# Kernel optimization log

Hardware: AMD Instinct MI355X
Metric: run time of the kernel (lower is better)

## Reference

```python
import jax, jax.numpy as jnp
import numpy as np
import math

B, S, D, H = 2, 2048, 1024, 16
DH = D // H
FF = 4096
EPS = 1e-5


def _xavier(k, shape):
    lim = math.sqrt(6.0 / (shape[0] + shape[1]))
    return jax.random.uniform(k, shape, jnp.float32, -lim, lim)


def setup_inputs() -> dict:
    key = jax.random.key(0)
    ks = jax.random.split(key, 8)
    return {
        "x": jax.random.normal(ks[0], (B, S, D), jnp.float32),
        "mask": jnp.ones((B, S), jnp.int32),
        "WQ": _xavier(ks[1], (D, D)), "bQ": jnp.zeros((D,), jnp.float32),
        "WK": _xavier(ks[2], (D, D)), "bK": jnp.zeros((D,), jnp.float32),
        "WV": _xavier(ks[3], (D, D)), "bV": jnp.zeros((D,), jnp.float32),
        "WY": _xavier(ks[4], (D, D)), "bY": jnp.zeros((D,), jnp.float32),
        "ln1_w": jnp.ones((D,), jnp.float32), "ln1_b": jnp.zeros((D,), jnp.float32),
        "ln2_w": jnp.ones((D,), jnp.float32), "ln2_b": jnp.zeros((D,), jnp.float32),
        "W1": _xavier(ks[5], (D, FF)), "b1": jnp.zeros((FF,), jnp.float32),
        "W2": _xavier(ks[6], (FF, D)), "b2": jnp.zeros((D,), jnp.float32),
    }


def _layer_norm(x, w, b):
    # manual LayerNorm: biased variance over last dim
    m = jnp.mean(x, axis=-1, keepdims=True)
    v = jnp.mean(jnp.square(x - m), axis=-1, keepdims=True)
    return (x - m) / jnp.sqrt(v + EPS) * w + b


def _attention(x, mask, WQ, bQ, WK, bK, WV, bV, WY, bY):
    b, s, _ = x.shape
    def split(t):  # (B,S,D) -> (B,H,S,DH)
        return t.reshape(b, s, H, DH).transpose(0, 2, 1, 3)
    q = split(x @ WQ + bQ)
    k = split(x @ WK + bK)
    v = split(x @ WV + bV)
    scores = jnp.einsum('bhqd,bhkd->bhqk', q, k) / math.sqrt(DH)
    scores = jnp.where(mask[:, None, None, :] == 0, -jnp.inf, scores)
    w = jax.nn.softmax(scores, axis=-1)
    y = jnp.einsum('bhqk,bhkd->bhqd', w, v)
    y = y.transpose(0, 2, 1, 3).reshape(b, s, D)  # merge heads
    return y @ WY + bY


def reference(x, mask, WQ, bQ, WK, bK, WV, bV, WY, bY,
              ln1_w, ln1_b, ln2_w, ln2_b, W1, b1, W2, b2):
    a = _attention(x, mask, WQ, bQ, WK, bK, WV, bV, WY, bY)
    h = _layer_norm(a + x, ln1_w, ln1_b)
    ff = jax.nn.gelu(h @ W1 + b1, approximate=False) @ W2 + b2
    return _layer_norm(ff + h, ln2_w, ln2_b)
```

## Files before the change

### kernel.cpp

```cpp
#include <hip/hip_runtime.h>
#include <cstdint>
#include <cstddef>

#define B_ 2
#define S_ 2048
#define D_ 1024
#define H_ 16
#define DH_ 64
#define FF_ 4096
#define M_ (B_*S_)
#define MB_ ((size_t)1 << 20)
#define NT_ (S_/64)

using u16 = unsigned short;
using u64 = unsigned long long;
using short8 = __attribute__((ext_vector_type(8))) short;
using short4v = __attribute__((ext_vector_type(4))) short;
using floatx4 = __attribute__((ext_vector_type(4))) float;
using u64x2 = __attribute__((ext_vector_type(2))) unsigned long long;

__device__ __forceinline__ float bf2f(u16 u) {
    return __uint_as_float(((uint32_t)u) << 16);
}
__device__ __forceinline__ u16 f2bf(float f) {
    uint32_t u = __float_as_uint(f);
    u += 0x7fffu + ((u >> 16) & 1u);
    return (u16)(u >> 16);
}
__device__ __forceinline__ uint32_t cvtpk_bf16(float lo, float hi) {
    uint32_t r;
    asm("v_cvt_pk_bf16_f32 %0, %1, %2" : "=v"(r) : "v"(lo), "v"(hi));
    return r;
}
__device__ __forceinline__ void async_copy16(const u16* g, u16* l) {
    __builtin_amdgcn_global_load_lds(
        (const __attribute__((address_space(1))) uint32_t*)g,
        (__attribute__((address_space(3))) uint32_t*)l, 16, 0, 0);
}

__device__ __forceinline__ float gelu_f(float v) {
    const float ax = fabsf(v) * 0.70710678118f;
    const float t  = __builtin_amdgcn_rcpf(fmaf(0.3275911f, ax, 1.f));
    float p = fmaf(1.061405429f, t, -1.453152027f);
    p = fmaf(p, t, 1.421413741f);
    p = fmaf(p, t, -0.284496736f);
    p = fmaf(p, t, 0.254829592f);
    p *= t;
    const float e = __builtin_amdgcn_exp2f(ax * ax * -1.4426950408889634f);
    float erfv = fmaf(-p, e, 1.f);
    erfv = copysignf(erfv, v);
    return 0.5f * v * (1.f + erfv);
}

__device__ __forceinline__ int swz_inv(int l) {
    return (l & 56) | ((l - (l >> 3)) & 7);
}
__device__ __forceinline__ int swz_fwd(int b) {
    return (b & 56) | ((b + (b >> 3)) & 7);
}

__device__ __forceinline__ void stage4(const u16* gA, const u16* gB,
                                       u16* lA, u16* lB, int w, int K) {
    async_copy16(gA, lA + w * 512);
    async_copy16(gA + (size_t)64 * K, lA + w * 512 + 2048);
    async_copy16(gB, lB + w * 512);
    async_copy16(gB + (size_t)64 * K, lB + w * 512 + 2048);
}

__device__ __forceinline__ void gemm_core(
    const u16* gA, const u16* gB, int K, int nk,
    u16 (&As)[3][128 * 32], u16 (&Bs)[3][128 * 32],
    int w, int wm, int wn, int lm, int quad, floatx4 (&acc)[4][4])
{
    const int pblk = swz_fwd(lm * 4 + quad);

    stage4(gA, gB, As[0], Bs[0], w, K); gA += 32; gB += 32;
    stage4(gA, gB, As[1], Bs[1], w, K); gA += 32; gB += 32;
    asm volatile("s_waitcnt vmcnt(4)" ::: "memory");
    __builtin_amdgcn_s_barrier();

    int cur = 0, stg = 2;
    for (int t = 0; t < nk; ++t) {
        if (t + 2 < nk) {
            stage4(gA, gB, As[stg], Bs[stg], w, K);
            gA += 32; gB += 32;
        }
        const u16* Ac = As[cur];
        const u16* Bc = Bs[cur];
        short8 af[4], bfr[4];
#pragma unroll
        for (int t4 = 0; t4 < 4; ++t4)
            af[t4] = *(const short8*)&Ac[(wm * 4 + t4) * 512 + pblk * 8];
#pragma unroll
        for (int t4 = 0; t4 < 4; ++t4)
            bfr[t4] = *(const short8*)&Bc[(wn * 4 + t4) * 512 + pblk * 8];
#pragma unroll
        for (int i = 0; i < 4; ++i)
#pragma unroll
            for (int j = 0; j < 4; ++j)
                acc[i][j] = __builtin_amdgcn_mfma_f32_16x16x32_bf16(
                    af[i], bfr[j], acc[i][j], 0, 0, 0);

        if (t + 2 < nk)      asm volatile("s_waitcnt vmcnt(4)" ::: "memory");
        else if (t + 1 < nk) asm volatile("s_waitcnt vmcnt(0)" ::: "memory");
        if (t + 1 < nk) __builtin_amdgcn_s_barrier();
        cur = (cur == 2) ? 0 : cur + 1;
        stg = (stg == 2) ? 0 : stg + 1;
    }
}

__global__ __launch_bounds__(256) void cvt_f32_bf16(
    const float* __restrict__ in, u16* __restrict__ out, int n)
{
    const int i = (blockIdx.x * 256 + threadIdx.x) * 4;
    if (i < n) {
        const float4 v = *(const float4*)(in + i);
        out[i + 0] = f2bf(v.x);
        out[i + 1] = f2bf(v.y);
        out[i + 2] = f2bf(v.z);
        out[i + 3] = f2bf(v.w);
    }
}

__global__ __launch_bounds__(256) void mask_bias(
    const int* __restrict__ mask, float* __restrict__ bias, int n)
{
    const int i = blockIdx.x * 256 + threadIdx.x;
    if (i < n) bias[i] = mask[i] ? 0.f : -1e30f;
}

__global__ void transpose_cvt(const float* __restrict__ in, u16* __restrict__ out,
                              int R, int C) {
    __shared__ float t[32][33];
    const int bx = blockIdx.x * 32, by = blockIdx.y * 32;
    const int tx = threadIdx.x, ty = threadIdx.y;
#pragma unroll
    for (int i = 0; i < 32; i += 8)
        t[ty + i][tx] = in[(size_t)(by + ty + i) * C + bx + tx];
    __syncthreads();
#pragma unroll
    for (int i = 0; i < 32; i += 8)
        out[(size_t)(bx + ty + i) * R + by + tx] = f2bf(t[tx][ty + i]);
}

__global__ void transpose_cvt4(
    const float* __restrict__ WQ, const float* __restrict__ WK,
    const float* __restrict__ WV, const float* __restrict__ WY,
    u16* __restrict__ Wqkvt, u16* __restrict__ WYt)
{
    __shared__ float t[32][33];
    const int zz = blockIdx.z;
    const float* in = zz == 0 ? WQ : zz == 1 ? WK : zz == 2 ? WV : WY;
    u16* out = zz < 3 ? Wqkvt + (size_t)zz * D_ * D_ : WYt;
    const int bx = blockIdx.x * 32, by = blockIdx.y * 32;
    const int tx = threadIdx.x, ty = threadIdx.y;
#pragma unroll
    for (int i = 0; i < 32; i += 8)
        t[ty + i][tx] = in[(size_t)(by + ty + i) * D_ + bx + tx];
    __syncthreads();
#pragma unroll
    for (int i = 0; i < 32; i += 8)
        out[(size_t)(bx + ty + i) * D_ + by + tx] = f2bf(t[tx][ty + i]);
}

template<bool GELU, bool OUT_F32>
__global__ __launch_bounds__(256) void gemm_bt(
    const u16* __restrict__ A, const u16* __restrict__ Bt,
    const float* __restrict__ bias, void* __restrict__ Cout,
    int M, int N, int K)
{
    __shared__ alignas(16) u16 As[3][128 * 32];
    __shared__ alignas(16) u16 Bs[3][128 * 32];
    const int tid = threadIdx.x;
    const int w = tid >> 6, lane = tid & 63;
    const int lm = lane & 15, quad = lane >> 4;
    const int wm = w >> 1, wn = w & 1;

    const int nwg = gridDim.x * gridDim.y;
    int bid = blockIdx.y * gridDim.x + blockIdx.x;
    if ((nwg & 7) == 0) {
        const int cpx = nwg >> 3;
        bid = (bid & 7) * cpx + (bid >> 3);
    }
    const int bx = bid % gridDim.x, by = bid / gridDim.x;
    const size_t m0 = (size_t)by * 128, n0 = (size_t)bx * 128;

    const int bwr = swz_inv(lane);
    const int rowS = w * 16 + (bwr >> 2);
    const int colS = (bwr & 3) * 8;
    const u16* gA = A + (m0 + rowS) * K + colS;
    const u16* gB = Bt + (n0 + rowS) * K + colS;

    floatx4 acc[4][4];
    const floatx4 z = {0.f, 0.f, 0.f, 0.f};
#pragma unroll
    for (int i = 0; i < 4; ++i)
#pragma unroll
        for (int j = 0; j < 4; ++j) acc[i][j] = z;

    gemm_core(gA, gB, K, K >> 5, As, Bs, w, wm, wn, lm, quad, acc);

#pragma unroll
    for (int i = 0; i < 4; ++i) {
        const size_t r0 = m0 + wm * 64 + i * 16 + quad * 4;
#pragma unroll
        for (int j = 0; j < 4; ++j) {
            const size_t c = n0 + wn * 64 + j * 16 + lm;
            const float bv = bias[c];
#pragma unroll
            for (int t = 0; t < 4; ++t) {
                float v = acc[i][j][t] + bv;
                if (GELU) v = gelu_f(v);
                if (OUT_F32) ((float*)Cout)[(r0 + t) * (size_t)N + c] = v;
                else         ((u16*)Cout)[(r0 + t) * (size_t)N + c] = f2bf(v);
            }
        }
    }
}

__global__ __launch_bounds__(256) void gemm_bt_skp(
    const u16* __restrict__ A, const u16* __restrict__ Bt,
    const float* __restrict__ bias, float* __restrict__ out0,
    float* __restrict__ Pext, int M, int N, int K)
{
    __shared__ alignas(16) u16 As[3][128 * 32];
    __shared__ alignas(16) u16 Bs[3][128 * 32];
    const int tid = threadIdx.x;
    const int w = tid >> 6, lane = tid & 63;
    const int lm = lane & 15, quad = lane >> 4;
    const int wm = w >> 1, wn = w & 1;
    const int kh = blockIdx.z;
    const int Ks = K / gridDim.z;

    const int nwg = gridDim.x * gridDim.y;
    int bid = blockIdx.y * gridDim.x + blockIdx.x;
    if ((nwg & 7) == 0) {
        const int cpx = nwg >> 3;
        bid = (bid & 7) * cpx + (bid >> 3);
    }
    const int bx = bid % gridDim.x, by = bid / gridDim.x;
    const size_t m0 = (size_t)by * 128, n0 = (size_t)bx * 128;

    const int bwr = swz_inv(lane);
    const int rowS = w * 16 + (bwr >> 2);
    const int colS = (bwr & 3) * 8;
    const u16* gA = A + (m0 + rowS) * K + (size_t)kh * Ks + colS;
    const u16* gB = Bt + (n0 + rowS) * K + (size_t)kh * Ks + colS;

    floatx4 acc[4][4];
    const floatx4 z = {0.f, 0.f, 0.f, 0.f};
#pragma unroll
    for (int i = 0; i < 4; ++i)
#pragma unroll
        for (int j = 0; j < 4; ++j) acc[i][j] = z;

    gemm_core(gA, gB, K, Ks >> 5, As, Bs, w, wm, wn, lm, quad, acc);

    float* Cout = (kh == 0) ? out0 : Pext + (size_t)(kh - 1) * ((size_t)M * N);
#pragma unroll
    for (int i = 0; i < 4; ++i) {
        const size_t r0 = m0 + wm * 64 + i * 16 + quad * 4;
#pragma unroll
        for (int j = 0; j < 4; ++j) {
            const size_t c = n0 + wn * 64 + j * 16 + lm;
            const float bv = (kh == 0) ? bias[c] : 0.f;
#pragma unroll
            for (int t = 0; t < 4; ++t)
                Cout[(r0 + t) * (size_t)N + c] = acc[i][j][t] + bv;
        }
    }
}

__global__ __launch_bounds__(256) void gemm_bt_sk2(
    const u16* __restrict__ A, const u16* __restrict__ Bt,
    const float* __restrict__ bias, float* __restrict__ Cout,
    int M, int N, int K)
{
    __shared__ alignas(16) u16 As[3][128 * 32];
    __shared__ alignas(16) u16 Bs[3][128 * 32];
    const int tid = threadIdx.x;
    const int w = tid >> 6, lane = tid & 63;
    const int lm = lane & 15, quad = lane >> 4;
    const int wm = w >> 1, wn = w & 1;
    const int kh = blockIdx.z;
    const int Ks = K >> 1;
    const size_t m0 = (size_t)blockIdx.y * 128, n0 = (size_t)blockIdx.x * 128;

    const int bwr = swz_inv(lane);
    const int rowS = w * 16 + (bwr >> 2);
    const int colS = (bwr & 3) * 8;
    const u16* gA = A + (m0 + rowS) * K + (size_t)kh * Ks + colS;
    const u16* gB = Bt + (n0 + rowS) * K + (size_t)kh * Ks + colS;

    floatx4 acc[4][4];
    const floatx4 z = {0.f, 0.f, 0.f, 0.f};
#pragma unroll
    for (int i = 0; i < 4; ++i)
#pragma unroll
        for (int j = 0; j < 4; ++j) acc[i][j] = z;

    gemm_core(gA, gB, K, Ks >> 5, As, Bs, w, wm, wn, lm, quad, acc);

#pragma unroll
    for (int i = 0; i < 4; ++i) {
        const size_t r0 = m0 + wm * 64 + i * 16 + quad * 4;
#pragma unroll
        for (int j = 0; j < 4; ++j) {
            const size_t c = n0 + wn * 64 + j * 16 + lm;
            const float bv = (kh == 0) ? bias[c] : 0.f;
#pragma unroll
            for (int t = 0; t < 4; ++t)
                atomicAdd(&Cout[(r0 + t) * (size_t)N + c], acc[i][j][t] + bv);
        }
    }
}

__global__ __launch_bounds__(256) void gemm_qkv(
    const u16* __restrict__ A, const u16* __restrict__ Bt,
    const float* __restrict__ bQ, const float* __restrict__ bK,
    const float* __restrict__ bV,
    u16* __restrict__ Qb, u16* __restrict__ Kb, u16* __restrict__ Vt)
{
    const int K = D_;
    __shared__ alignas(16) u16 As[3][128 * 32];
    __shared__ alignas(16) u16 Bs[3][128 * 32];
    const int tid = threadIdx.x;
    const int w = tid >> 6, lane = tid & 63;
    const int lm = lane & 15, quad = lane >> 4;
    const int wm = w >> 1, wn = w & 1;

    const int nwg = gridDim.x * gridDim.y;
    int bid = blockIdx.y * gridDim.x + blockIdx.x;
    if ((nwg & 7) == 0) {
        const int cpx = nwg >> 3;
        bid = (bid & 7) * cpx + (bid >> 3);
    }
    const int bx = bid % gridDim.x, by = bid / gridDim.x;
    const size_t m0 = (size_t)by * 128, n0 = (size_t)bx * 128;

    const int bwr = swz_inv(lane);
    const int rowS = w * 16 + (bwr >> 2);
    const int colS = (bwr & 3) * 8;
    const u16* gA = A + (m0 + rowS) * K + colS;
    const u16* gB = Bt + (n0 + rowS) * K + colS;

    floatx4 acc[4][4];
    const floatx4 z = {0.f, 0.f, 0.f, 0.f};
#pragma unroll
    for (int i = 0; i < 4; ++i)
#pragma unroll
        for (int j = 0; j < 4; ++j) acc[i][j] = z;

    gemm_core(gA, gB, K, K >> 5, As, Bs, w, wm, wn, lm, quad, acc);

#pragma unroll
    for (int i = 0; i < 4; ++i) {
        const size_t r0 = m0 + wm * 64 + i * 16 + quad * 4;
#pragma unroll
        for (int j = 0; j < 4; ++j) {
            const size_t c = n0 + wn * 64 + j * 16 + lm;
            const int sel = (int)(c >> 10);
            const int col = (int)(c & 1023);
            const float bv = sel == 0 ? bQ[col] : (sel == 1 ? bK[col] : bV[col]);
#pragma unroll
            for (int t = 0; t < 4; ++t) {
                const size_t r = r0 + t;
                const u16 v = f2bf(acc[i][j][t] + bv);
                if (sel == 0)      Qb[r * (size_t)D_ + col] = v;
                else if (sel == 1) Kb[r * (size_t)D_ + col] = v;
                else {
                    const int h = col >> 6, dh = col & 63;
                    const int bb = (int)(r >> 11), s = (int)(r & 2047);
                    Vt[((size_t)((bb * 16 + h) * 64 + dh)) * S_ + s] = v;
                }
            }
        }
    }
}

__global__ __launch_bounds__(256) void attn_kernel(
    const u16* __restrict__ Q, const u16* __restrict__ Kg,
    const u16* __restrict__ Vt, const float* __restrict__ mbias,
    u16* __restrict__ O)
{
    __shared__ alignas(16) u16 Kt[2][64 * 72];
    __shared__ alignas(16) u16 Vs[2][64 * 72];
    const int tid = threadIdx.x, w = tid >> 6, lane = tid & 63;
    const int lm = lane & 15, quad = lane >> 4;
    const int b = blockIdx.y >> 4, h = blockIdx.y & 15;
    const int q0 = blockIdx.x * 64;

    const u16* qp = Q + ((size_t)(b * S_ + q0 + w * 16 + lm)) * D_ + h * 64;
    const short8 bq0 = *(const short8*)(qp + quad * 8);
    const short8 bq1 = *(const short8*)(qp + 32 + quad * 8);

    const int sRow = tid >> 2, sCol = (tid & 3) * 16;
    const int wswz = (sRow & 8) ? 4 : 0;
    const int vswz = (lane & 8) ? 4 : 0;
    const u16* gK = Kg + ((size_t)(b * S_ + sRow)) * D_ + h * 64 + sCol;
    const u16* gV = Vt + ((size_t)((b * 16 + h) * 64 + sRow)) * S_ + sCol;

    float mrow = -1e30f, lrow = 0.f;
    floatx4 o[4];
    const floatx4 z = {0.f, 0.f, 0.f, 0.f};
#pragma unroll
    for (int i = 0; i < 4; ++i) o[i] = z;

    const float* bp = mbias + b * S_;
    const float SCL = 0.18033688011112042f;

    short8 rk0 = *(const short8*)(gK);
    short8 rk1 = *(const short8*)(gK + 8);
    short8 rv0 = *(const short8*)(gV);
    short8 rv1 = *(const short8*)(gV + 8);

    for (int it = 0; it < NT_; ++it) {
        u16* kb = Kt[it & 1];
        u16* vb = Vs[it & 1];
        *(short8*)&kb[sRow * 72 + sCol]     = rk0;
        *(short8*)&kb[sRow * 72 + sCol + 8] = rk1;
        {
            const u64x2 v0 = __builtin_bit_cast(u64x2, rv0);
            const u64x2 v1 = __builtin_bit_cast(u64x2, rv1);
            *(u64*)&vb[sRow * 72 + ((sCol     ) ^ wswz)] = v0[0];
            *(u64*)&vb[sRow * 72 + ((sCol + 4 ) ^ wswz)] = v0[1];
            *(u64*)&vb[sRow * 72 + ((sCol + 8 ) ^ wswz)] = v1[0];
            *(u64*)&vb[sRow * 72 + ((sCol + 12) ^ wswz)] = v1[1];
        }
        __syncthreads();
        if (it + 1 < NT_) {
            gK += (size_t)64 * D_; gV += 64;
            rk0 = *(const short8*)(gK);
            rk1 = *(const short8*)(gK + 8);
            rv0 = *(const short8*)(gV);
            rv1 = *(const short8*)(gV + 8);
        }

        floatx4 st[4];
        __builtin_amdgcn_s_setprio(1);
#pragma unroll
        for (int ks = 0; ks < 4; ++ks) {
            floatx4 s = z;
            const short8 ak0 = *(const short8*)&kb[(ks * 16 + lm) * 72 + quad * 8];
            const short8 ak1 = *(const short8*)&kb[(ks * 16 + lm) * 72 + 32 + quad * 8];
            s = __builtin_amdgcn_mfma_f32_16x16x32_bf16(ak0, bq0, s, 0, 0, 0);
            s = __builtin_amdgcn_mfma_f32_16x16x32_bf16(ak1, bq1, s, 0, 0, 0);
            const float4 mb4 = *(const float4*)&bp[it * 64 + ks * 16 + quad * 4];
            st[ks][0] = fmaf(s[0], SCL, mb4.x);
            st[ks][1] = fmaf(s[1], SCL, mb4.y);
            st[ks][2] = fmaf(s[2], SCL, mb4.z);
            st[ks][3] = fmaf(s[3], SCL, mb4.w);
        }
        __builtin_amdgcn_s_setprio(0);

        float m01 = fmaxf(fmaxf(st[0][0], st[0][1]), fmaxf(st[0][2], st[0][3]));
        float m11 = fmaxf(fmaxf(st[1][0], st[1][1]), fmaxf(st[1][2], st[1][3]));
        float m21 = fmaxf(fmaxf(st[2][0], st[2][1]), fmaxf(st[2][2], st[2][3]));
        float m31 = fmaxf(fmaxf(st[3][0], st[3][1]), fmaxf(st[3][2], st[3][3]));
        float tm = fmaxf(fmaxf(m01, m11), fmaxf(m21, m31));
        tm = fmaxf(tm, __shfl_xor(tm, 16));
        tm = fmaxf(tm, __shfl_xor(tm, 32));

        if (!__all(tm <= mrow + 8.f)) {
            const float mn = fmaxf(mrow, tm);
            const float al = __builtin_amdgcn_exp2f(mrow - mn);
            mrow = mn;
            lrow *= al;
#pragma unroll
            for (int d = 0; d < 4; ++d) o[d] *= al;
        }

        float sks[4];
#pragma unroll
        for (int ks = 0; ks < 4; ++ks) {
#pragma unroll
            for (int r = 0; r < 4; ++r)
                st[ks][r] = __builtin_amdgcn_exp2f(st[ks][r] - mrow);
            sks[ks] = (st[ks][0] + st[ks][1]) + (st[ks][2] + st[ks][3]);
        }
        float rs = (sks[0] + sks[1]) + (sks[2] + sks[3]);
        rs += __shfl_xor(rs, 16);
        rs += __shfl_xor(rs, 32);
        lrow += rs;

        short4v pb[4];
#pragma unroll
        for (int ks = 0; ks < 4; ++ks) {
            uint2 uu;
            uu.x = cvtpk_bf16(st[ks][0], st[ks][1]);
            uu.y = cvtpk_bf16(st[ks][2], st[ks][3]);
            pb[ks] = __builtin_bit_cast(short4v, uu);
        }
        __builtin_amdgcn_s_setprio(1);
#pragma unroll
        for (int d = 0; d < 4; ++d)
#pragma unroll
            for (int ks = 0; ks < 4; ++ks) {
                const short4v av = *(const short4v*)
                    &vb[(d * 16 + lm) * 72 + ((ks * 16 + quad * 4) ^ vswz)];
                o[d] = __builtin_amdgcn_mfma_f32_16x16x16bf16_1k(av, pb[ks], o[d], 0, 0, 0);
            }
        __builtin_amdgcn_s_setprio(0);
    }
    const float inv = __builtin_amdgcn_rcpf(lrow);
    u16* op = O + ((size_t)(b * S_ + q0 + w * 16 + lm)) * D_ + h * 64 + quad * 4;
#pragma unroll
    for (int d = 0; d < 4; ++d) {
        uint2 uu;
        uu.x = cvtpk_bf16(o[d][0] * inv, o[d][1] * inv);
        uu.y = cvtpk_bf16(o[d][2] * inv, o[d][3] * inv);
        *(uint2*)(op + d * 16) = uu;
    }
}

template<bool MAIN_F32, bool RESID_F32, bool OUT_F32>
__global__ __launch_bounds__(256) void add_ln(
    const void* __restrict__ mainp, const void* __restrict__ resid,
    const float* __restrict__ gamma, const float* __restrict__ beta,
    void* __restrict__ out)
{
    const int row = blockIdx.x;
    const size_t base = (size_t)row * D_;
    const int t = threadIdx.x;
    const int w = t >> 6, lane = t & 63;
    float v[4];
#pragma unroll
    for (int i = 0; i < 4; ++i) {
        const int c = i * 256 + t;
        const float mv = MAIN_F32 ? ((const float*)mainp)[base + c]
                                  : bf2f(((const u16*)mainp)[base + c]);
        const float rv = RESID_F32 ? ((const float*)resid)[base + c]
                                   : bf2f(((const u16*)resid)[base + c]);
        v[i] = mv + rv;
    }
    float s = v[0] + v[1] + v[2] + v[3];
#pragma unroll
    for (int off = 32; off >= 1; off >>= 1) s += __shfl_xor(s, off);
    __shared__ float red[8];
    if (lane == 0) red[w] = s;
    __syncthreads();
    const float mean = (red[0] + red[1] + red[2] + red[3]) * (1.0f / D_);
    float q = 0.f;
#pragma unroll
    for (int i = 0; i < 4; ++i) { const float dd = v[i] - mean; q += dd * dd; }
#pragma unroll
    for (int off = 32; off >= 1; off >>= 1) q += __shfl_xor(q, off);
    if (lane == 0) red[4 + w] = q;
    __syncthreads();
    const float var = (red[4] + red[5] + red[6] + red[7]) * (1.0f / D_);
    const float rstd = rsqrtf(var + 1e-5f);
#pragma unroll
    for (int i = 0; i < 4; ++i) {
        const int c = i * 256 + t;
        const float o = (v[i] - mean) * rstd * gamma[c] + beta[c];
        if (OUT_F32) ((float*)out)[base + c] = o;
        else         ((u16*)out)[base + c] = f2bf(o);
    }
}

template<int NEXT, bool RESID_F32, bool OUT_F32>
__global__ __launch_bounds__(256) void add_ln_red(
    const float* __restrict__ mainp, const float* __restrict__ Pext,
    const void* __restrict__ resid,
    const float* __restrict__ gamma, const float* __restrict__ beta,
    void* __restrict__ out)
{
    const int row = blockIdx.x;
    const size_t base = (size_t)row * D_;
    const int t = threadIdx.x;
    const int w = t >> 6, lane = t & 63;
    float v[4];
#pragma unroll
    for (int i = 0; i < 4; ++i) {
        const int c = i * 256 + t;
        float s = mainp[base + c];
#pragma unroll
        for (int p = 0; p < NEXT; ++p)
            s += Pext[(size_t)p * ((size_t)M_ * D_) + base + c];
        s += RESID_F32 ? ((const float*)resid)[base + c]
                       : bf2f(((const u16*)resid)[base + c]);
        v[i] = s;
    }
    float s = v[0] + v[1] + v[2] + v[3];
#pragma unroll
    for (int off = 32; off >= 1; off >>= 1) s += __shfl_xor(s, off);
    __shared__ float red[8];
    if (lane == 0) red[w] = s;
    __syncthreads();
    const float mean = (red[0] + red[1] + red[2] + red[3]) * (1.0f / D_);
    float q = 0.f;
#pragma unroll
    for (int i = 0; i < 4; ++i) { const float dd = v[i] - mean; q += dd * dd; }
#pragma unroll
    for (int off = 32; off >= 1; off >>= 1) q += __shfl_xor(q, off);
    if (lane == 0) red[4 + w] = q;
    __syncthreads();
    const float var = (red[4] + red[5] + red[6] + red[7]) * (1.0f / D_);
    const float rstd = rsqrtf(var + 1e-5f);
#pragma unroll
    for (int i = 0; i < 4; ++i) {
        const int c = i * 256 + t;
        const float o = (v[i] - mean) * rstd * gamma[c] + beta[c];
        if (OUT_F32) ((float*)out)[base + c] = o;
        else         ((u16*)out)[base + c] = f2bf(o);
    }
}

extern "C" void kernel_launch(void* const* d_in, const int* in_sizes, int n_in,
                              void* d_out, int out_size, void* d_ws, size_t ws_size,
                              hipStream_t stream)
{
    const float* x   = (const float*)d_in[0];
    const int* mask  = (const int*)d_in[1];
    const float* WQ = (const float*)d_in[2];  const float* bQ = (const float*)d_in[3];
    const float* WK = (const float*)d_in[4];  const float* bK = (const float*)d_in[5];
    const float* WV = (const float*)d_in[6];  const float* bV = (const float*)d_in[7];
    const float* WY = (const float*)d_in[8];  const float* bY = (const float*)d_in[9];
    const float* ln1w = (const float*)d_in[10]; const float* ln1b = (const float*)d_in[11];
    const float* ln2w = (const float*)d_in[12]; const float* ln2b = (const float*)d_in[13];
    const float* W1 = (const float*)d_in[14]; const float* b1 = (const float*)d_in[15];
    const float* W2 = (const float*)d_in[16]; const float* b2 = (const float*)d_in[17];

    char* ws = (char*)d_ws;
    u16* xb    = (u16*)(ws + 0  * MB_);
    u16* Wqkvt = (u16*)(ws + 8  * MB_);
    u16* WYt   = (u16*)(ws + 14 * MB_);
    u16* Qb    = (u16*)(ws + 16 * MB_);
    u16* Kb    = (u16*)(ws + 24 * MB_);
    u16* Vt    = (u16*)(ws + 32 * MB_);
    u16* Yat   = (u16*)(ws + 40 * MB_);
    float* Ypf = (float*)(ws + 16 * MB_);
    u16* hbf   = (u16*)(ws + 8  * MB_);
    u16* W1t   = (u16*)(ws + 0  * MB_);
    u16* G     = (u16*)(ws + 16 * MB_);
    u16* W2t   = (u16*)(ws + 0  * MB_);
    float* mb  = (float*)(ws + 48 * MB_);
    float* Pext = (float*)(ws + 49 * MB_);

    const size_t PART = (size_t)M_ * D_ * sizeof(float);
    const bool ws1 = ws_size >= 49 * MB_ + 1 * PART;

    const dim3 tb(32, 8);

    cvt_f32_bf16<<<(M_*D_)/1024, 256, 0, stream>>>(x, xb, M_*D_);
    mask_bias<<<(B_*S_)/256, 256, 0, stream>>>(mask, mb, B_*S_);
    transpose_cvt4<<<dim3(D_/32, D_/32, 4), tb, 0, stream>>>(WQ, WK, WV, WY, Wqkvt, WYt);

    gemm_qkv<<<dim3(3*D_/128, M_/128), 256, 0, stream>>>(xb, Wqkvt, bQ, bK, bV, Qb, Kb, Vt);

    attn_kernel<<<dim3(S_/64, B_*H_), 256, 0, stream>>>(Qb, Kb, Vt, mb, Yat);

    if (ws1) {
        gemm_bt_skp<<<dim3(D_/128, M_/128, 2), 256, 0, stream>>>(
            Yat, WYt, bY, Ypf, Pext, M_, D_, D_);
        add_ln_red<1,true,false><<<M_, 256, 0, stream>>>(Ypf, Pext, x, ln1w, ln1b, hbf);
    } else {
        hipMemsetAsync(Ypf, 0, PART, stream);
        gemm_bt_sk2<<<dim3(D_/128, M_/128, 2), 256, 0, stream>>>(
            Yat, WYt, bY, Ypf, M_, D_, D_);
        add_ln<true,true,false><<<M_, 256, 0, stream>>>(Ypf, x, ln1w, ln1b, hbf);
    }

    transpose_cvt<<<dim3(FF_/32, D_/32), tb, 0, stream>>>(W1, W1t, D_, FF_);
    gemm_bt<true,false><<<dim3(FF_/128, M_/128), 256, 0, stream>>>(hbf, W1t, b1, G, M_, FF_, D_);

    transpose_cvt<<<dim3(D_/32, FF_/32), tb, 0, stream>>>(W2, W2t, FF_, D_);

    if (ws1) {
        gemm_bt_skp<<<dim3(D_/128, M_/128, 2), 256, 0, stream>>>(
            G, W2t, b2, (float*)d_out, Pext, M_, D_, FF_);
        add_ln_red<1,false,true><<<M_, 256, 0, stream>>>(
            (float*)d_out, Pext, hbf, ln2w, ln2b, d_out);
    } else {
        hipMemsetAsync(d_out, 0, (size_t)M_ * D_ * 4, stream);
        gemm_bt_sk2<<<dim3(D_/128, M_/128, 2), 256, 0, stream>>>(
            G, W2t, b2, (float*)d_out, M_, D_, FF_);
        add_ln<true,false,true><<<M_, 256, 0, stream>>>(
            (float*)d_out, hbf, ln2w, ln2b, d_out);
    }
}
```

Measured before the change: 399.6 us.

## Enlarge GEMM tiles to 256x256 with 512 threads and split-K by four

All GEMM kernels move from 128x128 tiles with 4 waves to 256x256 tiles with 8 waves, each wave holding a 128x64 accumulator. The XOR-style LDS swizzle is dropped in favour of a plain row-major staging layout. When the workspace is large enough, the output-projection and FF2 GEMMs split K four ways, with a matching reduction in the add+layernorm kernel. The goal is more data reuse per block and fewer global loads per flop. The cost is 96KB of LDS per block, more register pressure, fewer blocks (the QKV grid drops below the CU count) and possible LDS bank conflicts from the unswizzled reads.

```diff
diff --git a/kernel.cpp b/kernel.cpp
--- a/kernel.cpp
+++ b/kernel.cpp
@@ -52,50 +52,41 @@
     return 0.5f * v * (1.f + erfv);
 }
 
-__device__ __forceinline__ int swz_inv(int l) {
-    return (l & 56) | ((l - (l >> 3)) & 7);
-}
-__device__ __forceinline__ int swz_fwd(int b) {
-    return (b & 56) | ((b + (b >> 3)) & 7);
-}
-
-__device__ __forceinline__ void stage4(const u16* gA, const u16* gB,
+__device__ __forceinline__ void stage8(const u16* gA, const u16* gB,
                                        u16* lA, u16* lB, int w, int K) {
-    async_copy16(gA, lA + w * 512);
-    async_copy16(gA + (size_t)64 * K, lA + w * 512 + 2048);
-    async_copy16(gB, lB + w * 512);
-    async_copy16(gB + (size_t)64 * K, lB + w * 512 + 2048);
-}
-
-__device__ __forceinline__ void gemm_core(
+    async_copy16(gA,                  lA + w * 1024);
+    async_copy16(gA + (size_t)16 * K, lA + w * 1024 + 512);
+    async_copy16(gB,                  lB + w * 1024);
+    async_copy16(gB + (size_t)16 * K, lB + w * 1024 + 512);
+}
+
+__device__ __forceinline__ void gemm_core256(
     const u16* gA, const u16* gB, int K, int nk,
-    u16 (&As)[3][128 * 32], u16 (&Bs)[3][128 * 32],
-    int w, int wm, int wn, int lm, int quad, floatx4 (&acc)[4][4])
-{
-    const int pblk = swz_fwd(lm * 4 + quad);
-
-    stage4(gA, gB, As[0], Bs[0], w, K); gA += 32; gB += 32;
-    stage4(gA, gB, As[1], Bs[1], w, K); gA += 32; gB += 32;
+    u16 (&As)[3][8192], u16 (&Bs)[3][8192],
+    int w, int wm, int wn, int lm, int quad, floatx4 (&acc)[8][4])
+{
+    stage8(gA, gB, As[0], Bs[0], w, K); gA += 32; gB += 32;
+    stage8(gA, gB, As[1], Bs[1], w, K); gA += 32; gB += 32;
     asm volatile("s_waitcnt vmcnt(4)" ::: "memory");
     __builtin_amdgcn_s_barrier();
 
     int cur = 0, stg = 2;
     for (int t = 0; t < nk; ++t) {
         if (t + 2 < nk) {
-            stage4(gA, gB, As[stg], Bs[stg], w, K);
+            stage8(gA, gB, As[stg], Bs[stg], w, K);
             gA += 32; gB += 32;
         }
         const u16* Ac = As[cur];
         const u16* Bc = Bs[cur];
-        short8 af[4], bfr[4];
-#pragma unroll
-        for (int t4 = 0; t4 < 4; ++t4)
-            af[t4] = *(const short8*)&Ac[(wm * 4 + t4) * 512 + pblk * 8];
-#pragma unroll
-        for (int t4 = 0; t4 < 4; ++t4)
-            bfr[t4] = *(const short8*)&Bc[(wn * 4 + t4) * 512 + pblk * 8];
-#pragma unroll
-        for (int i = 0; i < 4; ++i)
+        short8 af[8], bfr[4];
+#pragma unroll
+        for (int i = 0; i < 8; ++i)
+            af[i] = *(const short8*)&Ac[(wm * 128 + i * 16 + lm) * 32 + quad * 8];
+#pragma unroll
+        for (int j = 0; j < 4; ++j)
+            bfr[j] = *(const short8*)&Bc[(wn * 64 + j * 16 + lm) * 32 + quad * 8];
+#pragma unroll
+        for (int i = 0; i < 8; ++i)
 #pragma unroll
             for (int j = 0; j < 4; ++j)
                 acc[i][j] = __builtin_amdgcn_mfma_f32_16x16x32_bf16(
@@ -108,6 +99,17 @@
         stg = (stg == 2) ? 0 : stg + 1;
     }
 }
+
+struct G256 {
+    int w, lane, lm, quad, wm, wn, rowS, colS;
+    __device__ __forceinline__ G256(int tid) {
+        w = tid >> 6; lane = tid & 63;
+        lm = lane & 15; quad = lane >> 4;
+        wm = w >> 2; wn = w & 3;
+        rowS = w * 32 + (lane >> 2);
+        colS = (lane & 3) * 8;
+    }
+};
 
 __global__ __launch_bounds__(256) void cvt_f32_bf16(
     const float* __restrict__ in, u16* __restrict__ out, int n)
@@ -164,17 +166,14 @@
 }
 
 template<bool GELU, bool OUT_F32>
-__global__ __launch_bounds__(256) void gemm_bt(
+__global__ __launch_bounds__(512, 2) void gemm_bt(
     const u16* __restrict__ A, const u16* __restrict__ Bt,
     const float* __restrict__ bias, void* __restrict__ Cout,
     int M, int N, int K)
 {
-    __shared__ alignas(16) u16 As[3][128 * 32];
-    __shared__ alignas(16) u16 Bs[3][128 * 32];
-    const int tid = threadIdx.x;
-    const int w = tid >> 6, lane = tid & 63;
-    const int lm = lane & 15, quad = lane >> 4;
-    const int wm = w >> 1, wn = w & 1;
+    __shared__ alignas(16) u16 As[3][8192];
+    __shared__ alignas(16) u16 Bs[3][8192];
+    const G256 g(threadIdx.x);
 
     const int nwg = gridDim.x * gridDim.y;
     int bid = blockIdx.y * gridDim.x + blockIdx.x;
@@ -183,29 +182,26 @@
         bid = (bid & 7) * cpx + (bid >> 3);
     }
     const int bx = bid % gridDim.x, by = bid / gridDim.x;
-    const size_t m0 = (size_t)by * 128, n0 = (size_t)bx * 128;
-
-    const int bwr = swz_inv(lane);
-    const int rowS = w * 16 + (bwr >> 2);
-    const int colS = (bwr & 3) * 8;
-    const u16* gA = A + (m0 + rowS) * K + colS;
-    const u16* gB = Bt + (n0 + rowS) * K + colS;
-
-    floatx4 acc[4][4];
+    const size_t m0 = (size_t)by * 256, n0 = (size_t)bx * 256;
+
+    const u16* gA = A + (m0 + g.rowS) * K + g.colS;
+    const u16* gB = Bt + (n0 + g.rowS) * K + g.colS;
+
+    floatx4 acc[8][4];
     const floatx4 z = {0.f, 0.f, 0.f, 0.f};
 #pragma unroll
-    for (int i = 0; i < 4; ++i)
+    for (int i = 0; i < 8; ++i)
 #pragma unroll
         for (int j = 0; j < 4; ++j) acc[i][j] = z;
 
-    gemm_core(gA, gB, K, K >> 5, As, Bs, w, wm, wn, lm, quad, acc);
-
-#pragma unroll
-    for (int i = 0; i < 4; ++i) {
-        const size_t r0 = m0 + wm * 64 + i * 16 + quad * 4;
+    gemm_core256(gA, gB, K, K >> 5, As, Bs, g.w, g.wm, g.wn, g.lm, g.quad, acc);
+
+#pragma unroll
+    for (int i = 0; i < 8; ++i) {
+        const size_t r0 = m0 + g.wm * 128 + i * 16 + g.quad * 4;
 #pragma unroll
         for (int j = 0; j < 4; ++j) {
-            const size_t c = n0 + wn * 64 + j * 16 + lm;
+            const size_t c = n0 + g.wn * 64 + j * 16 + g.lm;
             const float bv = bias[c];
 #pragma unroll
             for (int t = 0; t < 4; ++t) {
@@ -218,17 +214,14 @@
     }
 }
 
-__global__ __launch_bounds__(256) void gemm_bt_skp(
+__global__ __launch_bounds__(512, 2) void gemm_bt_skp(
     const u16* __restrict__ A, const u16* __restrict__ Bt,
     const float* __restrict__ bias, float* __restrict__ out0,
     float* __restrict__ Pext, int M, int N, int K)
 {
-    __shared__ alignas(16) u16 As[3][128 * 32];
-    __shared__ alignas(16) u16 Bs[3][128 * 32];
-    const int tid = threadIdx.x;
-    const int w = tid >> 6, lane = tid & 63;
-    const int lm = lane & 15, quad = lane >> 4;
-    const int wm = w >> 1, wn = w & 1;
+    __shared__ alignas(16) u16 As[3][8192];
+    __shared__ alignas(16) u16 Bs[3][8192];
+    const G256 g(threadIdx.x);
     const int kh = blockIdx.z;
     const int Ks = K / gridDim.z;
 
@@ -239,30 +232,27 @@
         bid = (bid & 7) * cpx + (bid >> 3);
     }
     const int bx = bid % gridDim.x, by = bid / gridDim.x;
-    const size_t m0 = (size_t)by * 128, n0 = (size_t)bx * 128;
-
-    const int bwr = swz_inv(lane);
-    const int rowS = w * 16 + (bwr >> 2);
-    const int colS = (bwr & 3) * 8;
-    const u16* gA = A + (m0 + rowS) * K + (size_t)kh * Ks + colS;
-    const u16* gB = Bt + (n0 + rowS) * K + (size_t)kh * Ks + colS;
-
-    floatx4 acc[4][4];
+    const size_t m0 = (size_t)by * 256, n0 = (size_t)bx * 256;
+
+    const u16* gA = A + (m0 + g.rowS) * K + (size_t)kh * Ks + g.colS;
+    const u16* gB = Bt + (n0 + g.rowS) * K + (size_t)kh * Ks + g.colS;
+
+    floatx4 acc[8][4];
     const floatx4 z = {0.f, 0.f, 0.f, 0.f};
 #pragma unroll
-    for (int i = 0; i < 4; ++i)
+    for (int i = 0; i < 8; ++i)
 #pragma unroll
         for (int j = 0; j < 4; ++j) acc[i][j] = z;
 
-    gemm_core(gA, gB, K, Ks >> 5, As, Bs, w, wm, wn, lm, quad, acc);
+    gemm_core256(gA, gB, K, Ks >> 5, As, Bs, g.w, g.wm, g.wn, g.lm, g.quad, acc);
 
     float* Cout = (kh == 0) ? out0 : Pext + (size_t)(kh - 1) * ((size_t)M * N);
 #pragma unroll
-    for (int i = 0; i < 4; ++i) {
-        const size_t r0 = m0 + wm * 64 + i * 16 + quad * 4;
+    for (int i = 0; i < 8; ++i) {
+        const size_t r0 = m0 + g.wm * 128 + i * 16 + g.quad * 4;
 #pragma unroll
         for (int j = 0; j < 4; ++j) {
-            const size_t c = n0 + wn * 64 + j * 16 + lm;
+            const size_t c = n0 + g.wn * 64 + j * 16 + g.lm;
             const float bv = (kh == 0) ? bias[c] : 0.f;
 #pragma unroll
             for (int t = 0; t < 4; ++t)
@@ -271,42 +261,36 @@
     }
 }
 
-__global__ __launch_bounds__(256) void gemm_bt_sk2(
+__global__ __launch_bounds__(512, 2) void gemm_bt_sk2(
     const u16* __restrict__ A, const u16* __restrict__ Bt,
     const float* __restrict__ bias, float* __restrict__ Cout,
     int M, int N, int K)
 {
-    __shared__ alignas(16) u16 As[3][128 * 32];
-    __shared__ alignas(16) u16 Bs[3][128 * 32];
-    const int tid = threadIdx.x;
-    const int w = tid >> 6, lane = tid & 63;
-    const int lm = lane & 15, quad = lane >> 4;
-    const int wm = w >> 1, wn = w & 1;
+    __shared__ alignas(16) u16 As[3][8192];
+    __shared__ alignas(16) u16 Bs[3][8192];
+    const G256 g(threadIdx.x);
     const int kh = blockIdx.z;
     const int Ks = K >> 1;
-    const size_t m0 = (size_t)blockIdx.y * 128, n0 = (size_t)blockIdx.x * 128;
-
-    const int bwr = swz_inv(lane);
-    const int rowS = w * 16 + (bwr >> 2);
-    const int colS = (bwr & 3) * 8;
-    const u16* gA = A + (m0 + rowS) * K + (size_t)kh * Ks + colS;
-    const u16* gB = Bt + (n0 + rowS) * K + (size_t)kh * Ks + colS;
-
-    floatx4 acc[4][4];
+    const size_t m0 = (size_t)blockIdx.y * 256, n0 = (size_t)blockIdx.x * 256;
+
+    const u16* gA = A + (m0 + g.rowS) * K + (size_t)kh * Ks + g.colS;
+    const u16* gB = Bt + (n0 + g.rowS) * K + (size_t)kh * Ks + g.colS;
+
+    floatx4 acc[8][4];
     const floatx4 z = {0.f, 0.f, 0.f, 0.f};
 #pragma unroll
-    for (int i = 0; i < 4; ++i)
+    for (int i = 0; i < 8; ++i)
 #pragma unroll
         for (int j = 0; j < 4; ++j) acc[i][j] = z;
 
-    gemm_core(gA, gB, K, Ks >> 5, As, Bs, w, wm, wn, lm, quad, acc);
-
-#pragma unroll
-    for (int i = 0; i < 4; ++i) {
-        const size_t r0 = m0 + wm * 64 + i * 16 + quad * 4;
+    gemm_core256(gA, gB, K, Ks >> 5, As, Bs, g.w, g.wm, g.wn, g.lm, g.quad, acc);
+
+#pragma unroll
+    for (int i = 0; i < 8; ++i) {
+        const size_t r0 = m0 + g.wm * 128 + i * 16 + g.quad * 4;
 #pragma unroll
         for (int j = 0; j < 4; ++j) {
-            const size_t c = n0 + wn * 64 + j * 16 + lm;
+            const size_t c = n0 + g.wn * 64 + j * 16 + g.lm;
             const float bv = (kh == 0) ? bias[c] : 0.f;
 #pragma unroll
             for (int t = 0; t < 4; ++t)
@@ -315,19 +299,16 @@
     }
 }
 
-__global__ __launch_bounds__(256) void gemm_qkv(
+__global__ __launch_bounds__(512, 2) void gemm_qkv(
     const u16* __restrict__ A, const u16* __restrict__ Bt,
     const float* __restrict__ bQ, const float* __restrict__ bK,
     const float* __restrict__ bV,
     u16* __restrict__ Qb, u16* __restrict__ Kb, u16* __restrict__ Vt)
 {
     const int K = D_;
-    __shared__ alignas(16) u16 As[3][128 * 32];
-    __shared__ alignas(16) u16 Bs[3][128 * 32];
-    const int tid = threadIdx.x;
-    const int w = tid >> 6, lane = tid & 63;
-    const int lm = lane & 15, quad = lane >> 4;
-    const int wm = w >> 1, wn = w & 1;
+    __shared__ alignas(16) u16 As[3][8192];
+    __shared__ alignas(16) u16 Bs[3][8192];
+    const G256 g(threadIdx.x);
 
     const int nwg = gridDim.x * gridDim.y;
     int bid = blockIdx.y * gridDim.x + blockIdx.x;
@@ -336,29 +317,26 @@
         bid = (bid & 7) * cpx + (bid >> 3);
     }
     const int bx = bid % gridDim.x, by = bid / gridDim.x;
-    const size_t m0 = (size_t)by * 128, n0 = (size_t)bx * 128;
-
-    const int bwr = swz_inv(lane);
-    const int rowS = w * 16 + (bwr >> 2);
-    const int colS = (bwr & 3) * 8;
-    const u16* gA = A + (m0 + rowS) * K + colS;
-    const u16* gB = Bt + (n0 + rowS) * K + colS;
-
-    floatx4 acc[4][4];
+    const size_t m0 = (size_t)by * 256, n0 = (size_t)bx * 256;
+
+    const u16* gA = A + (m0 + g.rowS) * K + g.colS;
+    const u16* gB = Bt + (n0 + g.rowS) * K + g.colS;
+
+    floatx4 acc[8][4];
     const floatx4 z = {0.f, 0.f, 0.f, 0.f};
 #pragma unroll
-    for (int i = 0; i < 4; ++i)
+    for (int i = 0; i < 8; ++i)
 #pragma unroll
         for (int j = 0; j < 4; ++j) acc[i][j] = z;
 
-    gemm_core(gA, gB, K, K >> 5, As, Bs, w, wm, wn, lm, quad, acc);
-
-#pragma unroll
-    for (int i = 0; i < 4; ++i) {
-        const size_t r0 = m0 + wm * 64 + i * 16 + quad * 4;
+    gemm_core256(gA, gB, K, K >> 5, As, Bs, g.w, g.wm, g.wn, g.lm, g.quad, acc);
+
+#pragma unroll
+    for (int i = 0; i < 8; ++i) {
+        const size_t r0 = m0 + g.wm * 128 + i * 16 + g.quad * 4;
 #pragma unroll
         for (int j = 0; j < 4; ++j) {
-            const size_t c = n0 + wn * 64 + j * 16 + lm;
+            const size_t c = n0 + g.wn * 64 + j * 16 + g.lm;
             const int sel = (int)(c >> 10);
             const int col = (int)(c & 1023);
             const float bv = sel == 0 ? bQ[col] : (sel == 1 ? bK[col] : bV[col]);
@@ -639,6 +617,7 @@
 
     const size_t PART = (size_t)M_ * D_ * sizeof(float);
     const bool ws1 = ws_size >= 49 * MB_ + 1 * PART;
+    const bool ws3 = ws_size >= 49 * MB_ + 3 * PART;
 
     const dim3 tb(32, 8);
 
@@ -646,34 +625,43 @@
     mask_bias<<<(B_*S_)/256, 256, 0, stream>>>(mask, mb, B_*S_);
     transpose_cvt4<<<dim3(D_/32, D_/32, 4), tb, 0, stream>>>(WQ, WK, WV, WY, Wqkvt, WYt);
 
-    gemm_qkv<<<dim3(3*D_/128, M_/128), 256, 0, stream>>>(xb, Wqkvt, bQ, bK, bV, Qb, Kb, Vt);
+    gemm_qkv<<<dim3(3*D_/256, M_/256), 512, 0, stream>>>(xb, Wqkvt, bQ, bK, bV, Qb, Kb, Vt);
 
     attn_kernel<<<dim3(S_/64, B_*H_), 256, 0, stream>>>(Qb, Kb, Vt, mb, Yat);
 
-    if (ws1) {
-        gemm_bt_skp<<<dim3(D_/128, M_/128, 2), 256, 0, stream>>>(
+    if (ws3) {
+        gemm_bt_skp<<<dim3(D_/256, M_/256, 4), 512, 0, stream>>>(
+            Yat, WYt, bY, Ypf, Pext, M_, D_, D_);
+        add_ln_red<3,true,false><<<M_, 256, 0, stream>>>(Ypf, Pext, x, ln1w, ln1b, hbf);
+    } else if (ws1) {
+        gemm_bt_skp<<<dim3(D_/256, M_/256, 2), 512, 0, stream>>>(
             Yat, WYt, bY, Ypf, Pext, M_, D_, D_);
         add_ln_red<1,true,false><<<M_, 256, 0, stream>>>(Ypf, Pext, x, ln1w, ln1b, hbf);
     } else {
         hipMemsetAsync(Ypf, 0, PART, stream);
-        gemm_bt_sk2<<<dim3(D_/128, M_/128, 2), 256, 0, stream>>>(
+        gemm_bt_sk2<<<dim3(D_/256, M_/256, 2), 512, 0, stream>>>(
             Yat, WYt, bY, Ypf, M_, D_, D_);
         add_ln<true,true,false><<<M_, 256, 0, stream>>>(Ypf, x, ln1w, ln1b, hbf);
     }
 
     transpose_cvt<<<dim3(FF_/32, D_/32), tb, 0, stream>>>(W1, W1t, D_, FF_);
-    gemm_bt<true,false><<<dim3(FF_/128, M_/128), 256, 0, stream>>>(hbf, W1t, b1, G, M_, FF_, D_);
+    gemm_bt<true,false><<<dim3(FF_/256, M_/256), 512, 0, stream>>>(hbf, W1t, b1, G, M_, FF_, D_);
 
     transpose_cvt<<<dim3(D_/32, FF_/32), tb, 0, stream>>>(W2, W2t, FF_, D_);
 
-    if (ws1) {
-        gemm_bt_skp<<<dim3(D_/128, M_/128, 2), 256, 0, stream>>>(
+    if (ws3) {
+        gemm_bt_skp<<<dim3(D_/256, M_/256, 4), 512, 0, stream>>>(
+            G, W2t, b2, (float*)d_out, Pext, M_, D_, FF_);
+        add_ln_red<3,false,true><<<M_, 256, 0, stream>>>(
+            (float*)d_out, Pext, hbf, ln2w, ln2b, d_out);
+    } else if (ws1) {
+        gemm_bt_skp<<<dim3(D_/256, M_/256, 2), 512, 0, stream>>>(
             G, W2t, b2, (float*)d_out, Pext, M_, D_, FF_);
         add_ln_red<1,false,true><<<M_, 256, 0, stream>>>(
             (float*)d_out, Pext, hbf, ln2w, ln2b, d_out);
     } else {
         hipMemsetAsync(d_out, 0, (size_t)M_ * D_ * 4, stream);
-        gemm_bt_sk2<<<dim3(D_/128, M_/128, 2), 256, 0, stream>>>(
+        gemm_bt_sk2<<<dim3(D_/256, M_/256, 2), 512, 0, stream>>>(
             G, W2t, b2, (float*)d_out, M_, D_, FF_);
         add_ln<true,false,true><<<M_, 256, 0, stream>>>(
             (float*)d_out, hbf, ln2w, ln2b, d_out);
```

Measured after the change: 435.2 us. 1.09x slower.
